# Performance work log

Hardware: AMD Instinct MI355X
Metric: run time of the kernel (lower is better)

Reference implementation:

```python
import jax, jax.numpy as jnp
import numpy as np

B, H = 65536, 128
NUM_LAW, NUM_ACCU, NUM_TIME = 103, 119, 11


def _lstm_cell(x, h, c, Wx, Wh, b):
    # Keras LSTMCell: gates ordered i, f, g, o along last dim of [*, 4H]
    z = x @ Wx + h @ Wh + b
    i, f, g, o = jnp.split(z, 4, axis=-1)
    c_new = jax.nn.sigmoid(f) * c + jax.nn.sigmoid(i) * jnp.tanh(g)
    h_new = jax.nn.sigmoid(o) * jnp.tanh(c_new)
    return h_new, c_new


def setup_inputs() -> dict:
    key = jax.random.key(0)
    ks = jax.random.split(key, 16)
    s = 0.05
    return {
        "x": jax.random.normal(ks[0], (B, H), jnp.float32),
        "Wx": jax.random.normal(ks[1], (3, H, 4 * H), jnp.float32) * s,
        "Wh": jax.random.normal(ks[2], (3, H, 4 * H), jnp.float32) * s,
        "b": jax.random.normal(ks[3], (3, 4 * H), jnp.float32) * s,
        "hfc_W": jax.random.normal(ks[4], (H, H), jnp.float32) * s,
        "hfc_b": jax.random.normal(ks[5], (H,), jnp.float32) * s,
        "cfc_W": jax.random.normal(ks[6], (H, H), jnp.float32) * s,
        "cfc_b": jax.random.normal(ks[7], (H,), jnp.float32) * s,
        "mid_W": jax.random.normal(ks[8], (3, H, H), jnp.float32) * s,
        "mid_b": jax.random.normal(ks[9], (3, H), jnp.float32) * s,
        "out1_W": jax.random.normal(ks[10], (H, NUM_LAW), jnp.float32) * s,
        "out1_b": jax.random.normal(ks[11], (NUM_LAW,), jnp.float32) * s,
        "out2_W": jax.random.normal(ks[12], (H, NUM_ACCU), jnp.float32) * s,
        "out2_b": jax.random.normal(ks[13], (NUM_ACCU,), jnp.float32) * s,
        "out3_W": jax.random.normal(ks[14], (H, NUM_TIME), jnp.float32) * s,
        "out3_b": jax.random.normal(ks[15], (NUM_TIME,), jnp.float32) * s,
    }


def reference(x, Wx, Wh, b, hfc_W, hfc_b, cfc_W, cfc_b, mid_W, mid_b,
              out1_W, out1_b, out2_W, out2_b, out3_W, out3_b):
    zeros = jnp.zeros((B, H), x.dtype)
    # task 1 (law): starts from zero state
    h1, c1 = _lstm_cell(x, zeros, zeros, Wx[0], Wh[0], b[0])
    # graph edges (1,2),(1,3): first visit -> state copied directly (no Dense)
    # task 2 (accu): state = (h1, c1)
    h2, c2 = _lstm_cell(x, h1, c1, Wx[1], Wh[1], b[1])
    # edge (2,3): non-first -> additive dense fusion into task-3 state
    h3_in = h1 + h2 @ hfc_W + hfc_b
    c3_in = c1 + c2 @ cfc_W + cfc_b
    # task 3 (time)
    h3, c3 = _lstm_cell(x, h3_in, c3_in, Wx[2], Wh[2], b[2])
    # more_fc=True head: outfc(relu(midfc(h)))
    o1 = jax.nn.relu(h1 @ mid_W[0] + mid_b[0]) @ out1_W + out1_b
    o2 = jax.nn.relu(h2 @ mid_W[1] + mid_b[1]) @ out2_W + out2_b
    o3 = jax.nn.relu(h3 @ mid_W[2] + mid_b[2]) @ out3_W + out3_b
    return (o1, o2, o3)
```

## Files before the change

### kernel.cpp

```cpp
#include <hip/hip_runtime.h>


#define L2E 1.4426950408889634f

typedef _Float16 half8 __attribute__((ext_vector_type(8)));
typedef float f32x4 __attribute__((ext_vector_type(4)));

#define FWX0 0
#define FWX1 8192
#define FWH1 16384
#define FWX2 24576
#define FWH2 32768
#define FHFC 40960
#define FCFC 43008
#define FMID0 45056
#define FMID1 47104
#define FMID2 49152
#define FOUT1 51200
#define FOUT2 52992
#define FOUT3 55040
#define NBLOB_F16 442368

__global__ void lstm_prep(const float* __restrict__ Wx, const float* __restrict__ Wh,
                          const float* __restrict__ hfcW, const float* __restrict__ cfcW,
                          const float* __restrict__ midW, const float* __restrict__ o1W,
                          const float* __restrict__ o2W, const float* __restrict__ o3W,
                          _Float16* __restrict__ blob)
{
    int idx = blockIdx.x * 256 + threadIdx.x;
    if (idx >= NBLOB_F16) return;

    const float* src;
    int style;
    int N = 0;
    int local;
    if      (idx < FWX1 * 8)  { src = Wx;           local = idx - FWX0 * 8;  style = 0; }
    else if (idx < FWH1 * 8)  { src = Wx + 65536;   local = idx - FWX1 * 8;  style = 0; }
    else if (idx < FWX2 * 8)  { src = Wh + 65536;   local = idx - FWH1 * 8;  style = 0; }
    else if (idx < FWH2 * 8)  { src = Wx + 131072;  local = idx - FWX2 * 8;  style = 0; }
    else if (idx < FHFC * 8)  { src = Wh + 131072;  local = idx - FWH2 * 8;  style = 0; }
    else if (idx < FCFC * 8)  { src = hfcW;         local = idx - FHFC * 8;  style = 1; }
    else if (idx < FMID0 * 8) { src = cfcW;         local = idx - FCFC * 8;  style = 1; }
    else if (idx < FMID1 * 8) { src = midW;         local = idx - FMID0 * 8; style = 1; }
    else if (idx < FMID2 * 8) { src = midW + 16384; local = idx - FMID1 * 8; style = 1; }
    else if (idx < FOUT1 * 8) { src = midW + 32768; local = idx - FMID2 * 8; style = 1; }
    else if (idx < FOUT2 * 8) { src = o1W;          local = idx - FOUT1 * 8; style = 2; N = 103; }
    else if (idx < FOUT3 * 8) { src = o2W;          local = idx - FOUT2 * 8; style = 2; N = 119; }
    else                      { src = o3W;          local = idx - FOUT3 * 8; style = 2; N = 11;  }

    int Mtile = local >> 11;
    int rem   = local & 2047;
    int kb    = rem >> 9;
    int lane  = (rem >> 3) & 63;
    int j     = rem & 7;
    int g = lane >> 4, m = lane & 15;
    int k = 32 * kb + ((j < 4) ? (4 * g + j) : (16 + 4 * g + (j - 4)));

    float v;
    if (style == 0) {
        int ft = Mtile >> 2, gate = Mtile & 3;
        int n = gate * 128 + ft * 16 + m;
        float s = (gate == 2) ? (2.0f * L2E) : (-L2E);
        v = src[k * 512 + n] * s;
    } else if (style == 1) {
        v = src[k * 128 + Mtile * 16 + m];
    } else {
        int n = Mtile * 16 + m;
        v = (n < N) ? src[k * N + n] : 0.0f;
    }
    blob[idx] = (_Float16)v;
}


__device__ __forceinline__ half8 ldA(const _Float16* __restrict__ blob, int base, int frag, int lane)
{
    return ((const half8*)blob)[base + frag * 64 + lane];
}

__device__ __forceinline__ half8 ldX(const float* __restrict__ xrow)
{
    const float4* p = (const float4*)xrow;
    float4 a = p[0];
    float4 b = p[4];
    half8 r;
    r[0] = (_Float16)a.x; r[1] = (_Float16)a.y; r[2] = (_Float16)a.z; r[3] = (_Float16)a.w;
    r[4] = (_Float16)b.x; r[5] = (_Float16)b.y; r[6] = (_Float16)b.z; r[7] = (_Float16)b.w;
    return r;
}

__device__ __forceinline__ float sigz(float z)
{
    return __builtin_amdgcn_rcpf(1.0f + __builtin_amdgcn_exp2f(z));
}

#define MFMA16(A, B, C) __builtin_amdgcn_mfma_f32_16x16x32_f16(A, B, C, 0, 0, 0)

__device__ __forceinline__ void stageA(const _Float16* __restrict__ blob, const float* __restrict__ b3,
                                       const half8 (&xf)[4], half8 (&ho)[4], half8 (&co)[4],
                                       int lane, int rowg)
{
#pragma unroll
    for (int ft = 0; ft < 8; ++ft) {
        f32x4 ai{0,0,0,0}, ag{0,0,0,0}, ao{0,0,0,0};
#pragma unroll
        for (int kb = 0; kb < 4; ++kb) {
            half8 A0 = ldA(blob, FWX0, (ft * 4 + 0) * 4 + kb, lane);
            half8 A2 = ldA(blob, FWX0, (ft * 4 + 2) * 4 + kb, lane);
            half8 A3 = ldA(blob, FWX0, (ft * 4 + 3) * 4 + kb, lane);
            ai = MFMA16(A0, xf[kb], ai);
            ag = MFMA16(A2, xf[kb], ag);
            ao = MFMA16(A3, xf[kb], ao);
        }
        float4 bi4 = *(const float4*)(b3 + 0   + ft * 16 + 4 * rowg);
        float4 bg4 = *(const float4*)(b3 + 256 + ft * 16 + 4 * rowg);
        float4 bo4 = *(const float4*)(b3 + 384 + ft * 16 + 4 * rowg);
        float bi[4] = {bi4.x, bi4.y, bi4.z, bi4.w};
        float bg[4] = {bg4.x, bg4.y, bg4.z, bg4.w};
        float bo[4] = {bo4.x, bo4.y, bo4.z, bo4.w};
#pragma unroll
        for (int r = 0; r < 4; ++r) {
            float si = sigz(ai[r] - L2E * bi[r]);
            float tg = 1.0f - 2.0f * sigz(ag[r] + 2.0f * L2E * bg[r]);
            float so = sigz(ao[r] - L2E * bo[r]);
            float c  = si * tg;
            float h  = so * (1.0f - 2.0f * sigz(2.0f * L2E * c));
            ho[ft >> 1][(ft & 1) * 4 + r] = (_Float16)h;
            co[ft >> 1][(ft & 1) * 4 + r] = (_Float16)c;
        }
    }
}

template <int L, bool WRITE_C>
__device__ __forceinline__ void zstage(const _Float16* __restrict__ blob, const float* __restrict__ b3,
                                       int FX, int FH,
                                       const half8 (&xf)[4], const half8 (&hf)[4],
                                       const half8 (&cp)[4],
                                       half8 (&ho)[4], half8 (&co)[4],
                                       int lane, int rowg)
{
#pragma unroll
    for (int ft = 0; ft < 8; ++ft) {
        f32x4 ai{0,0,0,0}, af{0,0,0,0}, ag{0,0,0,0}, ao{0,0,0,0};
#pragma unroll
        for (int kb = 0; kb < 4; ++kb) {
            half8 A0 = ldA(blob, FX, (ft * 4 + 0) * 4 + kb, lane);
            half8 A1 = ldA(blob, FX, (ft * 4 + 1) * 4 + kb, lane);
            half8 A2 = ldA(blob, FX, (ft * 4 + 2) * 4 + kb, lane);
            half8 A3 = ldA(blob, FX, (ft * 4 + 3) * 4 + kb, lane);
            ai = MFMA16(A0, xf[kb], ai);
            af = MFMA16(A1, xf[kb], af);
            ag = MFMA16(A2, xf[kb], ag);
            ao = MFMA16(A3, xf[kb], ao);
            half8 B0 = ldA(blob, FH, (ft * 4 + 0) * 4 + kb, lane);
            half8 B1 = ldA(blob, FH, (ft * 4 + 1) * 4 + kb, lane);
            half8 B2 = ldA(blob, FH, (ft * 4 + 2) * 4 + kb, lane);
            half8 B3 = ldA(blob, FH, (ft * 4 + 3) * 4 + kb, lane);
            ai = MFMA16(B0, hf[kb], ai);
            af = MFMA16(B1, hf[kb], af);
            ag = MFMA16(B2, hf[kb], ag);
            ao = MFMA16(B3, hf[kb], ao);
        }
        const float* bb = b3 + L * 512;
        float4 bi4 = *(const float4*)(bb + 0   + ft * 16 + 4 * rowg);
        float4 bf4 = *(const float4*)(bb + 128 + ft * 16 + 4 * rowg);
        float4 bg4 = *(const float4*)(bb + 256 + ft * 16 + 4 * rowg);
        float4 bo4 = *(const float4*)(bb + 384 + ft * 16 + 4 * rowg);
        float bi[4] = {bi4.x, bi4.y, bi4.z, bi4.w};
        float bf[4] = {bf4.x, bf4.y, bf4.z, bf4.w};
        float bg[4] = {bg4.x, bg4.y, bg4.z, bg4.w};
        float bo[4] = {bo4.x, bo4.y, bo4.z, bo4.w};
#pragma unroll
        for (int r = 0; r < 4; ++r) {
            float cprev = (float)cp[ft >> 1][(ft & 1) * 4 + r];
            float si = sigz(ai[r] - L2E * bi[r]);
            float sf = sigz(af[r] - L2E * bf[r]);
            float tg = 1.0f - 2.0f * sigz(ag[r] + 2.0f * L2E * bg[r]);
            float so = sigz(ao[r] - L2E * bo[r]);
            float c  = sf * cprev + si * tg;
            float h  = so * (1.0f - 2.0f * sigz(2.0f * L2E * c));
            ho[ft >> 1][(ft & 1) * 4 + r] = (_Float16)h;
            if (WRITE_C) co[ft >> 1][(ft & 1) * 4 + r] = (_Float16)c;
        }
    }
}

__device__ __forceinline__ void fcstage(const _Float16* __restrict__ blob, int FW,
                                        const float* __restrict__ fcb,
                                        const half8 (&bfr)[4], half8 (&io)[4],
                                        int lane, int rowg)
{
#pragma unroll
    for (int ft = 0; ft < 8; ++ft) {
        f32x4 acc{0,0,0,0};
#pragma unroll
        for (int kb = 0; kb < 4; ++kb) {
            half8 A = ldA(blob, FW, ft * 4 + kb, lane);
            acc = MFMA16(A, bfr[kb], acc);
        }
        float4 b4 = *(const float4*)(fcb + ft * 16 + 4 * rowg);
        float bbv[4] = {b4.x, b4.y, b4.z, b4.w};
#pragma unroll
        for (int r = 0; r < 4; ++r) {
            float v = acc[r] + bbv[r] + (float)io[ft >> 1][(ft & 1) * 4 + r];
            io[ft >> 1][(ft & 1) * 4 + r] = (_Float16)v;
        }
    }
}

template <int NMT>
__device__ __forceinline__ void head(const _Float16* __restrict__ blob, int FMID, int FOUT,
                                     const float* __restrict__ midb, const float* __restrict__ outb,
                                     int Nreal, float* __restrict__ outbase, int rowlen,
                                     const half8 (&hf)[4], half8 (&mfr)[4],
                                     int lane, int rowg, int col, int batch0)
{
#pragma unroll
    for (int ft = 0; ft < 8; ++ft) {
        f32x4 acc{0,0,0,0};
#pragma unroll
        for (int kb = 0; kb < 4; ++kb) {
            half8 A = ldA(blob, FMID, ft * 4 + kb, lane);
            acc = MFMA16(A, hf[kb], acc);
        }
        float4 b4 = *(const float4*)(midb + ft * 16 + 4 * rowg);
        float mb[4] = {b4.x, b4.y, b4.z, b4.w};
#pragma unroll
        for (int r = 0; r < 4; ++r) {
            float mv = fmaxf(acc[r] + mb[r], 0.0f);
            mfr[ft >> 1][(ft & 1) * 4 + r] = (_Float16)mv;
        }
    }
    int batch = batch0 + col;
#pragma unroll
    for (int Mt = 0; Mt < NMT; ++Mt) {
        f32x4 acc{0,0,0,0};
#pragma unroll
        for (int kb = 0; kb < 4; ++kb) {
            half8 A = ldA(blob, FOUT, Mt * 4 + kb, lane);
            acc = MFMA16(A, mfr[kb], acc);
        }
#pragma unroll
        for (int r = 0; r < 4; ++r) {
            int n = Mt * 16 + 4 * rowg + r;
            if (n < Nreal)
                outbase[batch * rowlen + n] = acc[r] + outb[n];
        }
    }
}

__global__ __launch_bounds__(256, 2) void lstm_fused(
    const float* __restrict__ x, const float* __restrict__ b3,
    const float* __restrict__ hfc_b, const float* __restrict__ cfc_b,
    const float* __restrict__ mid_b, const float* __restrict__ o1b,
    const float* __restrict__ o2b, const float* __restrict__ o3b,
    const _Float16* __restrict__ blob, float* __restrict__ out)
{
    int tid = threadIdx.x;
    int lane = tid & 63;
    int wv = tid >> 6;
    int wave = blockIdx.x * 4 + wv;
    int batch0 = wave * 16;
    int rowg = lane >> 4, col = lane & 15;

    half8 xf[4], hA[4], cA[4], hB[4], cB[4], mfr[4];

#pragma unroll
    for (int kb = 0; kb < 4; ++kb)
        xf[kb] = ldX(x + (size_t)(batch0 + col) * 128 + 32 * kb + 4 * rowg);

    stageA(blob, b3, xf, hA, cA, lane, rowg);
    head<7>(blob, FMID0, FOUT1, mid_b, o1b, 103, out, 103, hA, mfr, lane, rowg, col, batch0);
    zstage<1, true>(blob, b3, FWX1, FWH1, xf, hA, cA, hB, cB, lane, rowg);
    fcstage(blob, FHFC, hfc_b, hB, hA, lane, rowg);
    fcstage(blob, FCFC, cfc_b, cB, cA, lane, rowg);
    head<8>(blob, FMID1, FOUT2, mid_b + 128, o2b, 119, out + (size_t)65536 * 103, 119, hB, mfr, lane, rowg, col, batch0);
    zstage<2, false>(blob, b3, FWX2, FWH2, xf, hA, cA, hB, cB, lane, rowg);
    head<1>(blob, FMID2, FOUT3, mid_b + 256, o3b, 11, out + (size_t)65536 * 222, 11, hB, mfr, lane, rowg, col, batch0);
}

extern "C" void kernel_launch(void* const* d_in, const int* in_sizes, int n_in,
                              void* d_out, int out_size, void* d_ws, size_t ws_size,
                              hipStream_t stream)
{
    const float* x     = (const float*)d_in[0];
    const float* Wx    = (const float*)d_in[1];
    const float* Wh    = (const float*)d_in[2];
    const float* b3    = (const float*)d_in[3];
    const float* hfcW  = (const float*)d_in[4];
    const float* hfc_b = (const float*)d_in[5];
    const float* cfcW  = (const float*)d_in[6];
    const float* cfc_b = (const float*)d_in[7];
    const float* midW  = (const float*)d_in[8];
    const float* mid_b = (const float*)d_in[9];
    const float* o1W   = (const float*)d_in[10];
    const float* o1b   = (const float*)d_in[11];
    const float* o2W   = (const float*)d_in[12];
    const float* o2b   = (const float*)d_in[13];
    const float* o3W   = (const float*)d_in[14];
    const float* o3b   = (const float*)d_in[15];
    float* out = (float*)d_out;

    if (ws_size < (size_t)NBLOB_F16 * sizeof(_Float16)) return;
    _Float16* blob = (_Float16*)d_ws;

    lstm_prep<<<(NBLOB_F16 + 255) / 256, 256, 0, stream>>>(Wx, Wh, hfcW, cfcW, midW, o1W, o2W, o3W, blob);
    lstm_fused<<<1024, 256, 0, stream>>>(x, b3, hfc_b, cfc_b, mid_b, o1b, o2b, o3b, blob, out);
}
```

Measured before the change: 321.6 us.

## Switch to 32x32 MFMA and stream weights through double-buffered LDS

Moves all GEMMs from 16x16x32 to 32x32x16 MFMA tiles, with each wave handling 32 batch rows instead of 16, and re-lays out the fp16 weight blob to match. Weight fragments are no longer read from global memory by every wave. Instead they go through a 55-phase schedule that prefetches the next phase into a double-buffered LDS region with global_load_lds, separated by block barriers. This is meant to cut redundant global/L2 weight traffic and raise MFMA efficiency. The cost is a barrier per phase, heavy register use (launch bounds drop to 1 block per CU) and half as many blocks.

```diff
diff --git a/kernel.cpp b/kernel.cpp
--- a/kernel.cpp
+++ b/kernel.cpp
@@ -4,7 +4,7 @@
 #define L2E 1.4426950408889634f
 
 typedef _Float16 half8 __attribute__((ext_vector_type(8)));
-typedef float f32x4 __attribute__((ext_vector_type(4)));
+typedef float f32x16 __attribute__((ext_vector_type(16)));
 
 #define FWX0 0
 #define FWX1 8192
@@ -17,9 +17,13 @@
 #define FMID1 47104
 #define FMID2 49152
 #define FOUT1 51200
-#define FOUT2 52992
-#define FOUT3 55040
-#define NBLOB_F16 442368
+#define FOUT2 53248
+#define FOUT3 55296
+#define NBLOB_H8 55808
+#define NBLOB_F16 446464
+
+#define MFMA32(A, B, C) __builtin_amdgcn_mfma_f32_32x32x16_f16(A, B, C, 0, 0, 0)
+#define ZERO16 f32x16{0,0,0,0,0,0,0,0,0,0,0,0,0,0,0,0}
 
 __global__ void lstm_prep(const float* __restrict__ Wx, const float* __restrict__ Wh,
                           const float* __restrict__ hfcW, const float* __restrict__ cfcW,
@@ -30,252 +34,309 @@
     int idx = blockIdx.x * 256 + threadIdx.x;
     if (idx >= NBLOB_F16) return;
 
+    int frag = idx >> 9;
+    int rem  = idx & 511;
+    int lane = rem >> 3;
+    int j    = rem & 7;
+    int m    = lane & 31;
+    int g    = lane >> 5;
+    int kin  = (j & 3) + 8 * (j >> 2) + 4 * g;
+
     const float* src;
-    int style;
-    int N = 0;
-    int local;
-    if      (idx < FWX1 * 8)  { src = Wx;           local = idx - FWX0 * 8;  style = 0; }
-    else if (idx < FWH1 * 8)  { src = Wx + 65536;   local = idx - FWX1 * 8;  style = 0; }
-    else if (idx < FWX2 * 8)  { src = Wh + 65536;   local = idx - FWH1 * 8;  style = 0; }
-    else if (idx < FWH2 * 8)  { src = Wx + 131072;  local = idx - FWX2 * 8;  style = 0; }
-    else if (idx < FHFC * 8)  { src = Wh + 131072;  local = idx - FWH2 * 8;  style = 0; }
-    else if (idx < FCFC * 8)  { src = hfcW;         local = idx - FHFC * 8;  style = 1; }
-    else if (idx < FMID0 * 8) { src = cfcW;         local = idx - FCFC * 8;  style = 1; }
-    else if (idx < FMID1 * 8) { src = midW;         local = idx - FMID0 * 8; style = 1; }
-    else if (idx < FMID2 * 8) { src = midW + 16384; local = idx - FMID1 * 8; style = 1; }
-    else if (idx < FOUT1 * 8) { src = midW + 32768; local = idx - FMID2 * 8; style = 1; }
-    else if (idx < FOUT2 * 8) { src = o1W;          local = idx - FOUT1 * 8; style = 2; N = 103; }
-    else if (idx < FOUT3 * 8) { src = o2W;          local = idx - FOUT2 * 8; style = 2; N = 119; }
-    else                      { src = o3W;          local = idx - FOUT3 * 8; style = 2; N = 11;  }
-
-    int Mtile = local >> 11;
-    int rem   = local & 2047;
-    int kb    = rem >> 9;
-    int lane  = (rem >> 3) & 63;
-    int j     = rem & 7;
-    int g = lane >> 4, m = lane & 15;
-    int k = 32 * kb + ((j < 4) ? (4 * g + j) : (16 + 4 * g + (j - 4)));
+    int style, N = 0, lf;
+    if      (frag < 128) { src = Wx;            lf = frag;       style = 0; }
+    else if (frag < 256) { src = Wx + 65536;    lf = frag - 128; style = 0; }
+    else if (frag < 384) { src = Wh + 65536;    lf = frag - 256; style = 0; }
+    else if (frag < 512) { src = Wx + 131072;   lf = frag - 384; style = 0; }
+    else if (frag < 640) { src = Wh + 131072;   lf = frag - 512; style = 0; }
+    else if (frag < 672) { src = hfcW;          lf = frag - 640; style = 1; }
+    else if (frag < 704) { src = cfcW;          lf = frag - 672; style = 1; }
+    else if (frag < 736) { src = midW;          lf = frag - 704; style = 1; }
+    else if (frag < 768) { src = midW + 16384;  lf = frag - 736; style = 1; }
+    else if (frag < 800) { src = midW + 32768;  lf = frag - 768; style = 1; }
+    else if (frag < 832) { src = o1W;           lf = frag - 800; style = 2; N = 103; }
+    else if (frag < 864) { src = o2W;           lf = frag - 832; style = 2; N = 119; }
+    else                 { src = o3W;           lf = frag - 864; style = 2; N = 11;  }
 
     float v;
     if (style == 0) {
-        int ft = Mtile >> 2, gate = Mtile & 3;
-        int n = gate * 128 + ft * 16 + m;
+        int mt = lf >> 5, gate = (lf >> 3) & 3, kc = lf & 7;
+        int k = kc * 16 + kin;
+        int n = gate * 128 + mt * 32 + m;
         float s = (gate == 2) ? (2.0f * L2E) : (-L2E);
         v = src[k * 512 + n] * s;
     } else if (style == 1) {
-        v = src[k * 128 + Mtile * 16 + m];
+        int mt = lf >> 3, kc = lf & 7;
+        v = src[(kc * 16 + kin) * 128 + mt * 32 + m];
     } else {
-        int n = Mtile * 16 + m;
-        v = (n < N) ? src[k * N + n] : 0.0f;
+        int mt = lf >> 3, kc = lf & 7;
+        int n = mt * 32 + m;
+        v = (n < N) ? src[(kc * 16 + kin) * N + n] : 0.0f;
     }
     blob[idx] = (_Float16)v;
 }
 
 
-__device__ __forceinline__ half8 ldA(const _Float16* __restrict__ blob, int base, int frag, int lane)
-{
-    return ((const half8*)blob)[base + frag * 64 + lane];
-}
-
-__device__ __forceinline__ half8 ldX(const float* __restrict__ xrow)
-{
-    const float4* p = (const float4*)xrow;
-    float4 a = p[0];
-    float4 b = p[4];
-    half8 r;
-    r[0] = (_Float16)a.x; r[1] = (_Float16)a.y; r[2] = (_Float16)a.z; r[3] = (_Float16)a.w;
-    r[4] = (_Float16)b.x; r[5] = (_Float16)b.y; r[6] = (_Float16)b.z; r[7] = (_Float16)b.w;
-    return r;
-}
-
 __device__ __forceinline__ float sigz(float z)
 {
     return __builtin_amdgcn_rcpf(1.0f + __builtin_amdgcn_exp2f(z));
 }
 
-#define MFMA16(A, B, C) __builtin_amdgcn_mfma_f32_16x16x32_f16(A, B, C, 0, 0, 0)
-
-__device__ __forceinline__ void stageA(const _Float16* __restrict__ blob, const float* __restrict__ b3,
-                                       const half8 (&xf)[4], half8 (&ho)[4], half8 (&co)[4],
-                                       int lane, int rowg)
-{
-#pragma unroll
-    for (int ft = 0; ft < 8; ++ft) {
-        f32x4 ai{0,0,0,0}, ag{0,0,0,0}, ao{0,0,0,0};
-#pragma unroll
-        for (int kb = 0; kb < 4; ++kb) {
-            half8 A0 = ldA(blob, FWX0, (ft * 4 + 0) * 4 + kb, lane);
-            half8 A2 = ldA(blob, FWX0, (ft * 4 + 2) * 4 + kb, lane);
-            half8 A3 = ldA(blob, FWX0, (ft * 4 + 3) * 4 + kb, lane);
-            ai = MFMA16(A0, xf[kb], ai);
-            ag = MFMA16(A2, xf[kb], ag);
-            ao = MFMA16(A3, xf[kb], ao);
-        }
-        float4 bi4 = *(const float4*)(b3 + 0   + ft * 16 + 4 * rowg);
-        float4 bg4 = *(const float4*)(b3 + 256 + ft * 16 + 4 * rowg);
-        float4 bo4 = *(const float4*)(b3 + 384 + ft * 16 + 4 * rowg);
-        float bi[4] = {bi4.x, bi4.y, bi4.z, bi4.w};
-        float bg[4] = {bg4.x, bg4.y, bg4.z, bg4.w};
-        float bo[4] = {bo4.x, bo4.y, bo4.z, bo4.w};
-#pragma unroll
-        for (int r = 0; r < 4; ++r) {
-            float si = sigz(ai[r] - L2E * bi[r]);
-            float tg = 1.0f - 2.0f * sigz(ag[r] + 2.0f * L2E * bg[r]);
-            float so = sigz(ao[r] - L2E * bo[r]);
-            float c  = si * tg;
-            float h  = so * (1.0f - 2.0f * sigz(2.0f * L2E * c));
-            ho[ft >> 1][(ft & 1) * 4 + r] = (_Float16)h;
-            co[ft >> 1][(ft & 1) * 4 + r] = (_Float16)c;
-        }
-    }
-}
-
-template <int L, bool WRITE_C>
-__device__ __forceinline__ void zstage(const _Float16* __restrict__ blob, const float* __restrict__ b3,
-                                       int FX, int FH,
-                                       const half8 (&xf)[4], const half8 (&hf)[4],
-                                       const half8 (&cp)[4],
-                                       half8 (&ho)[4], half8 (&co)[4],
-                                       int lane, int rowg)
-{
-#pragma unroll
-    for (int ft = 0; ft < 8; ++ft) {
-        f32x4 ai{0,0,0,0}, af{0,0,0,0}, ag{0,0,0,0}, ao{0,0,0,0};
-#pragma unroll
-        for (int kb = 0; kb < 4; ++kb) {
-            half8 A0 = ldA(blob, FX, (ft * 4 + 0) * 4 + kb, lane);
-            half8 A1 = ldA(blob, FX, (ft * 4 + 1) * 4 + kb, lane);
-            half8 A2 = ldA(blob, FX, (ft * 4 + 2) * 4 + kb, lane);
-            half8 A3 = ldA(blob, FX, (ft * 4 + 3) * 4 + kb, lane);
-            ai = MFMA16(A0, xf[kb], ai);
-            af = MFMA16(A1, xf[kb], af);
-            ag = MFMA16(A2, xf[kb], ag);
-            ao = MFMA16(A3, xf[kb], ao);
-            half8 B0 = ldA(blob, FH, (ft * 4 + 0) * 4 + kb, lane);
-            half8 B1 = ldA(blob, FH, (ft * 4 + 1) * 4 + kb, lane);
-            half8 B2 = ldA(blob, FH, (ft * 4 + 2) * 4 + kb, lane);
-            half8 B3 = ldA(blob, FH, (ft * 4 + 3) * 4 + kb, lane);
-            ai = MFMA16(B0, hf[kb], ai);
-            af = MFMA16(B1, hf[kb], af);
-            ag = MFMA16(B2, hf[kb], ag);
-            ao = MFMA16(B3, hf[kb], ao);
-        }
-        const float* bb = b3 + L * 512;
-        float4 bi4 = *(const float4*)(bb + 0   + ft * 16 + 4 * rowg);
-        float4 bf4 = *(const float4*)(bb + 128 + ft * 16 + 4 * rowg);
-        float4 bg4 = *(const float4*)(bb + 256 + ft * 16 + 4 * rowg);
-        float4 bo4 = *(const float4*)(bb + 384 + ft * 16 + 4 * rowg);
-        float bi[4] = {bi4.x, bi4.y, bi4.z, bi4.w};
-        float bf[4] = {bf4.x, bf4.y, bf4.z, bf4.w};
-        float bg[4] = {bg4.x, bg4.y, bg4.z, bg4.w};
-        float bo[4] = {bo4.x, bo4.y, bo4.z, bo4.w};
-#pragma unroll
-        for (int r = 0; r < 4; ++r) {
-            float cprev = (float)cp[ft >> 1][(ft & 1) * 4 + r];
-            float si = sigz(ai[r] - L2E * bi[r]);
-            float sf = sigz(af[r] - L2E * bf[r]);
-            float tg = 1.0f - 2.0f * sigz(ag[r] + 2.0f * L2E * bg[r]);
-            float so = sigz(ao[r] - L2E * bo[r]);
-            float c  = sf * cprev + si * tg;
-            float h  = so * (1.0f - 2.0f * sigz(2.0f * L2E * c));
-            ho[ft >> 1][(ft & 1) * 4 + r] = (_Float16)h;
-            if (WRITE_C) co[ft >> 1][(ft & 1) * 4 + r] = (_Float16)c;
-        }
-    }
-}
-
-__device__ __forceinline__ void fcstage(const _Float16* __restrict__ blob, int FW,
-                                        const float* __restrict__ fcb,
-                                        const half8 (&bfr)[4], half8 (&io)[4],
-                                        int lane, int rowg)
-{
-#pragma unroll
-    for (int ft = 0; ft < 8; ++ft) {
-        f32x4 acc{0,0,0,0};
-#pragma unroll
-        for (int kb = 0; kb < 4; ++kb) {
-            half8 A = ldA(blob, FW, ft * 4 + kb, lane);
-            acc = MFMA16(A, bfr[kb], acc);
-        }
-        float4 b4 = *(const float4*)(fcb + ft * 16 + 4 * rowg);
-        float bbv[4] = {b4.x, b4.y, b4.z, b4.w};
-#pragma unroll
-        for (int r = 0; r < 4; ++r) {
-            float v = acc[r] + bbv[r] + (float)io[ft >> 1][(ft & 1) * 4 + r];
-            io[ft >> 1][(ft & 1) * 4 + r] = (_Float16)v;
-        }
-    }
-}
-
-template <int NMT>
-__device__ __forceinline__ void head(const _Float16* __restrict__ blob, int FMID, int FOUT,
-                                     const float* __restrict__ midb, const float* __restrict__ outb,
-                                     int Nreal, float* __restrict__ outbase, int rowlen,
-                                     const half8 (&hf)[4], half8 (&mfr)[4],
-                                     int lane, int rowg, int col, int batch0)
-{
-#pragma unroll
-    for (int ft = 0; ft < 8; ++ft) {
-        f32x4 acc{0,0,0,0};
-#pragma unroll
-        for (int kb = 0; kb < 4; ++kb) {
-            half8 A = ldA(blob, FMID, ft * 4 + kb, lane);
-            acc = MFMA16(A, hf[kb], acc);
-        }
-        float4 b4 = *(const float4*)(midb + ft * 16 + 4 * rowg);
-        float mb[4] = {b4.x, b4.y, b4.z, b4.w};
-#pragma unroll
-        for (int r = 0; r < 4; ++r) {
-            float mv = fmaxf(acc[r] + mb[r], 0.0f);
-            mfr[ft >> 1][(ft & 1) * 4 + r] = (_Float16)mv;
-        }
-    }
-    int batch = batch0 + col;
-#pragma unroll
-    for (int Mt = 0; Mt < NMT; ++Mt) {
-        f32x4 acc{0,0,0,0};
-#pragma unroll
-        for (int kb = 0; kb < 4; ++kb) {
-            half8 A = ldA(blob, FOUT, Mt * 4 + kb, lane);
-            acc = MFMA16(A, mfr[kb], acc);
-        }
-#pragma unroll
-        for (int r = 0; r < 4; ++r) {
-            int n = Mt * 16 + 4 * rowg + r;
-            if (n < Nreal)
-                outbase[batch * rowlen + n] = acc[r] + outb[n];
-        }
-    }
-}
-
-__global__ __launch_bounds__(256, 2) void lstm_fused(
+__device__ __forceinline__ void phase_of(int p, int& b, int& n)
+{
+    n = 16;
+    if (p < 8)        b = FWX0 + (p >> 1) * 2048 + (p & 1) * 1024;
+    else if (p < 10)  b = FMID0 + (p - 8) * 1024;
+    else if (p < 12)  b = FOUT1 + (p - 10) * 1024;
+    else if (p < 28) { int q = p - 12, mt = q >> 2, sb = q & 3;
+                       b = ((sb & 2) ? FWH1 : FWX1) + mt * 2048 + (sb & 1) * 1024; }
+    else if (p < 30)  b = FHFC + (p - 28) * 1024;
+    else if (p < 32)  b = FCFC + (p - 30) * 1024;
+    else if (p < 34)  b = FMID1 + (p - 32) * 1024;
+    else if (p < 36)  b = FOUT2 + (p - 34) * 1024;
+    else if (p < 52) { int q = p - 36, mt = q >> 2, sb = q & 3;
+                       b = ((sb & 2) ? FWH2 : FWX2) + mt * 2048 + (sb & 1) * 1024; }
+    else if (p < 54)  b = FMID2 + (p - 52) * 1024;
+    else if (p == 54) { b = FOUT3; n = 8; }
+    else             { b = 0; n = 0; }
+}
+
+__device__ __forceinline__ void stage_phase(const _Float16* __restrict__ blob, int base_h8, int nfrags,
+                                            _Float16* dst, int wv, int lane)
+{
+    const char* gbase = (const char*)((const half8*)blob + base_h8);
+    auto* d = (__attribute__((address_space(3))) char*)dst;
+#pragma unroll
+    for (int i = 0; i < 4; ++i) {
+        int f = i * 4 + wv;
+        if (f < nfrags) {
+            __builtin_amdgcn_global_load_lds(
+                (const __attribute__((address_space(1))) void*)(gbase + (size_t)(f * 64 + lane) * 16),
+                (__attribute__((address_space(3))) void*)(d + f * 1024), 16, 0, 0);
+        }
+    }
+}
+
+#define STEP_BEGIN { int nb_, nn_; phase_of(p + 1, nb_, nn_);                     \
+                     if (nn_) stage_phase(blob, nb_, nn_, lds + (cur ^ 1) * 8192, wv, lane); \
+                     const _Float16* Lb = lds + cur * 8192;
+#define STEP_END     __syncthreads(); cur ^= 1; ++p; }
+#define LDS_FRAG(fl) (((const half8*)Lb)[(fl) * 64 + lane])
+
+__global__ __launch_bounds__(256, 1) void lstm_fused(
     const float* __restrict__ x, const float* __restrict__ b3,
     const float* __restrict__ hfc_b, const float* __restrict__ cfc_b,
     const float* __restrict__ mid_b, const float* __restrict__ o1b,
     const float* __restrict__ o2b, const float* __restrict__ o3b,
     const _Float16* __restrict__ blob, float* __restrict__ out)
 {
-    int tid = threadIdx.x;
-    int lane = tid & 63;
-    int wv = tid >> 6;
-    int wave = blockIdx.x * 4 + wv;
-    int batch0 = wave * 16;
-    int rowg = lane >> 4, col = lane & 15;
-
-    half8 xf[4], hA[4], cA[4], hB[4], cB[4], mfr[4];
-
-#pragma unroll
-    for (int kb = 0; kb < 4; ++kb)
-        xf[kb] = ldX(x + (size_t)(batch0 + col) * 128 + 32 * kb + 4 * rowg);
-
-    stageA(blob, b3, xf, hA, cA, lane, rowg);
-    head<7>(blob, FMID0, FOUT1, mid_b, o1b, 103, out, 103, hA, mfr, lane, rowg, col, batch0);
-    zstage<1, true>(blob, b3, FWX1, FWH1, xf, hA, cA, hB, cB, lane, rowg);
-    fcstage(blob, FHFC, hfc_b, hB, hA, lane, rowg);
-    fcstage(blob, FCFC, cfc_b, cB, cA, lane, rowg);
-    head<8>(blob, FMID1, FOUT2, mid_b + 128, o2b, 119, out + (size_t)65536 * 103, 119, hB, mfr, lane, rowg, col, batch0);
-    zstage<2, false>(blob, b3, FWX2, FWH2, xf, hA, cA, hB, cB, lane, rowg);
-    head<1>(blob, FMID2, FOUT3, mid_b + 256, o3b, 11, out + (size_t)65536 * 222, 11, hB, mfr, lane, rowg, col, batch0);
+    __shared__ _Float16 lds[16384];
+
+    int tid = threadIdx.x, lane = tid & 63, wv = tid >> 6;
+    int g = lane >> 5;
+    int batch = blockIdx.x * 128 + wv * 32 + (lane & 31);
+
+    half8 xf[8], hA[8], cA[8], hB[8], cB[8], mfr[8];
+
+#pragma unroll
+    for (int kc = 0; kc < 8; ++kc) {
+        const float* xr = x + (size_t)batch * 128 + kc * 16 + 4 * g;
+        float4 a = *(const float4*)xr;
+        float4 b = *(const float4*)(xr + 8);
+        half8 v;
+        v[0]=(_Float16)a.x; v[1]=(_Float16)a.y; v[2]=(_Float16)a.z; v[3]=(_Float16)a.w;
+        v[4]=(_Float16)b.x; v[5]=(_Float16)b.y; v[6]=(_Float16)b.z; v[7]=(_Float16)b.w;
+        xf[kc] = v;
+    }
+
+    int p = 0, cur = 0;
+    { int b0, n0; phase_of(0, b0, n0); stage_phase(blob, b0, n0, lds, wv, lane); }
+    __syncthreads();
+
+    auto head_mid = [&](const half8 (&hf)[8], const float* midbp) {
+#pragma unroll
+        for (int g2 = 0; g2 < 2; ++g2) {
+            STEP_BEGIN
+#pragma unroll
+            for (int mtl = 0; mtl < 2; ++mtl) {
+                const int mt = 2 * g2 + mtl;
+                f32x16 acc = ZERO16;
+#pragma unroll
+                for (int kc = 0; kc < 8; ++kc) acc = MFMA32(LDS_FRAG(mtl * 8 + kc), hf[kc], acc);
+#pragma unroll
+                for (int t = 0; t < 4; ++t) {
+                    float4 B4 = *(const float4*)(midbp + mt * 32 + 8 * t + 4 * g);
+                    float bv[4] = {B4.x, B4.y, B4.z, B4.w};
+#pragma unroll
+                    for (int s = 0; s < 4; ++s) {
+                        const int q = 4 * t + s;
+                        float mv = fmaxf(acc[q] + bv[s], 0.0f);
+                        if (q < 8) mfr[2 * mt][q] = (_Float16)mv; else mfr[2 * mt + 1][q - 8] = (_Float16)mv;
+                    }
+                }
+            }
+            STEP_END
+        }
+    };
+
+    auto head_out2 = [&](int Nreal, float* obase, int rowlen, const float* outb) {
+#pragma unroll
+        for (int g2 = 0; g2 < 2; ++g2) {
+            STEP_BEGIN
+#pragma unroll
+            for (int mtl = 0; mtl < 2; ++mtl) {
+                const int mt = 2 * g2 + mtl;
+                f32x16 acc = ZERO16;
+#pragma unroll
+                for (int kc = 0; kc < 8; ++kc) acc = MFMA32(LDS_FRAG(mtl * 8 + kc), mfr[kc], acc);
+#pragma unroll
+                for (int t = 0; t < 4; ++t)
+#pragma unroll
+                    for (int s = 0; s < 4; ++s) {
+                        const int q = 4 * t + s;
+                        int n = mt * 32 + 8 * t + 4 * g + s;
+                        if (n < Nreal) obase[(size_t)batch * rowlen + n] = acc[q] + outb[n];
+                    }
+            }
+            STEP_END
+        }
+    };
+
+    auto fc_f = [&](const half8 (&bfr)[8], half8 (&io)[8], const float* fcb) {
+#pragma unroll
+        for (int g2 = 0; g2 < 2; ++g2) {
+            STEP_BEGIN
+#pragma unroll
+            for (int mtl = 0; mtl < 2; ++mtl) {
+                const int mt = 2 * g2 + mtl;
+                f32x16 acc = ZERO16;
+#pragma unroll
+                for (int kc = 0; kc < 8; ++kc) acc = MFMA32(LDS_FRAG(mtl * 8 + kc), bfr[kc], acc);
+#pragma unroll
+                for (int t = 0; t < 4; ++t) {
+                    float4 B4 = *(const float4*)(fcb + mt * 32 + 8 * t + 4 * g);
+                    float bv[4] = {B4.x, B4.y, B4.z, B4.w};
+#pragma unroll
+                    for (int s = 0; s < 4; ++s) {
+                        const int q = 4 * t + s;
+                        float prev = (q < 8) ? (float)io[2 * mt][q] : (float)io[2 * mt + 1][q - 8];
+                        float v = acc[q] + bv[s] + prev;
+                        if (q < 8) io[2 * mt][q] = (_Float16)v; else io[2 * mt + 1][q - 8] = (_Float16)v;
+                    }
+                }
+            }
+            STEP_END
+        }
+    };
+
+    auto zstage_f = [&](const half8 (&hf)[8], const half8 (&cp)[8],
+                        half8 (&ho)[8], half8 (&co)[8], const float* bb, bool writeC) {
+#pragma unroll
+        for (int mt = 0; mt < 4; ++mt) {
+            f32x16 ai = ZERO16, af = ZERO16, agg = ZERO16, ao = ZERO16;
+            STEP_BEGIN
+#pragma unroll
+            for (int kc = 0; kc < 8; ++kc) { ai = MFMA32(LDS_FRAG(kc), xf[kc], ai);
+                                             af = MFMA32(LDS_FRAG(8 + kc), xf[kc], af); }
+            STEP_END
+            STEP_BEGIN
+#pragma unroll
+            for (int kc = 0; kc < 8; ++kc) { agg = MFMA32(LDS_FRAG(kc), xf[kc], agg);
+                                             ao  = MFMA32(LDS_FRAG(8 + kc), xf[kc], ao); }
+            STEP_END
+            STEP_BEGIN
+#pragma unroll
+            for (int kc = 0; kc < 8; ++kc) { ai = MFMA32(LDS_FRAG(kc), hf[kc], ai);
+                                             af = MFMA32(LDS_FRAG(8 + kc), hf[kc], af); }
+            STEP_END
+            STEP_BEGIN
+#pragma unroll
+            for (int kc = 0; kc < 8; ++kc) { agg = MFMA32(LDS_FRAG(kc), hf[kc], agg);
+                                             ao  = MFMA32(LDS_FRAG(8 + kc), hf[kc], ao); }
+#pragma unroll
+            for (int t = 0; t < 4; ++t) {
+                float4 Bi = *(const float4*)(bb + 0   + mt * 32 + 8 * t + 4 * g);
+                float4 Bf = *(const float4*)(bb + 128 + mt * 32 + 8 * t + 4 * g);
+                float4 Bg = *(const float4*)(bb + 256 + mt * 32 + 8 * t + 4 * g);
+                float4 Bo = *(const float4*)(bb + 384 + mt * 32 + 8 * t + 4 * g);
+                float bi[4]={Bi.x,Bi.y,Bi.z,Bi.w}, bf[4]={Bf.x,Bf.y,Bf.z,Bf.w};
+                float bg[4]={Bg.x,Bg.y,Bg.z,Bg.w}, bo[4]={Bo.x,Bo.y,Bo.z,Bo.w};
+#pragma unroll
+                for (int s = 0; s < 4; ++s) {
+                    const int q = 4 * t + s;
+                    float cprev = (q < 8) ? (float)cp[2 * mt][q] : (float)cp[2 * mt + 1][q - 8];
+                    float si = sigz(ai[q] - L2E * bi[s]);
+                    float sf = sigz(af[q] - L2E * bf[s]);
+                    float tg = 1.0f - 2.0f * sigz(agg[q] + 2.0f * L2E * bg[s]);
+                    float so = sigz(ao[q] - L2E * bo[s]);
+                    float c  = sf * cprev + si * tg;
+                    float h  = so * (1.0f - 2.0f * sigz(2.0f * L2E * c));
+                    if (q < 8) ho[2 * mt][q] = (_Float16)h; else ho[2 * mt + 1][q - 8] = (_Float16)h;
+                    if (writeC) { if (q < 8) co[2 * mt][q] = (_Float16)c; else co[2 * mt + 1][q - 8] = (_Float16)c; }
+                }
+            }
+            STEP_END
+        }
+    };
+
+#pragma unroll
+    for (int mt = 0; mt < 4; ++mt) {
+        f32x16 ai = ZERO16, agg = ZERO16, ao = ZERO16;
+        STEP_BEGIN
+#pragma unroll
+        for (int kc = 0; kc < 8; ++kc) ai = MFMA32(LDS_FRAG(kc), xf[kc], ai);
+        STEP_END
+        STEP_BEGIN
+#pragma unroll
+        for (int kc = 0; kc < 8; ++kc) { agg = MFMA32(LDS_FRAG(kc), xf[kc], agg);
+                                         ao  = MFMA32(LDS_FRAG(8 + kc), xf[kc], ao); }
+#pragma unroll
+        for (int t = 0; t < 4; ++t) {
+            float4 Bi = *(const float4*)(b3 + 0   + mt * 32 + 8 * t + 4 * g);
+            float4 Bg = *(const float4*)(b3 + 256 + mt * 32 + 8 * t + 4 * g);
+            float4 Bo = *(const float4*)(b3 + 384 + mt * 32 + 8 * t + 4 * g);
+            float bi[4]={Bi.x,Bi.y,Bi.z,Bi.w}, bg[4]={Bg.x,Bg.y,Bg.z,Bg.w}, bo[4]={Bo.x,Bo.y,Bo.z,Bo.w};
+#pragma unroll
+            for (int s = 0; s < 4; ++s) {
+                const int q = 4 * t + s;
+                float si = sigz(ai[q] - L2E * bi[s]);
+                float tg = 1.0f - 2.0f * sigz(agg[q] + 2.0f * L2E * bg[s]);
+                float so = sigz(ao[q] - L2E * bo[s]);
+                float c  = si * tg;
+                float h  = so * (1.0f - 2.0f * sigz(2.0f * L2E * c));
+                if (q < 8) { hA[2 * mt][q] = (_Float16)h; cA[2 * mt][q] = (_Float16)c; }
+                else       { hA[2 * mt + 1][q - 8] = (_Float16)h; cA[2 * mt + 1][q - 8] = (_Float16)c; }
+            }
+        }
+        STEP_END
+    }
+
+    head_mid(hA, mid_b);
+    head_out2(103, out, 103, o1b);
+    zstage_f(hA, cA, hB, cB, b3 + 512, true);
+    fc_f(hB, hA, hfc_b);
+    fc_f(cB, cA, cfc_b);
+    head_mid(hB, mid_b + 128);
+    head_out2(119, out + (size_t)65536 * 103, 119, o2b);
+    zstage_f(hA, cA, hB, cB, b3 + 1024, false);
+    head_mid(hB, mid_b + 256);
+
+    STEP_BEGIN
+    {
+        f32x16 acc = ZERO16;
+#pragma unroll
+        for (int kc = 0; kc < 8; ++kc) acc = MFMA32(LDS_FRAG(kc), mfr[kc], acc);
+        float* obase = out + (size_t)65536 * 222;
+#pragma unroll
+        for (int t = 0; t < 4; ++t)
+#pragma unroll
+            for (int s = 0; s < 4; ++s) {
+                const int q = 4 * t + s;
+                int n = 8 * t + 4 * g + s;
+                if (n < 11) obase[(size_t)batch * 11 + n] = acc[q] + o3b[n];
+            }
+    }
+    STEP_END
 }
 
 extern "C" void kernel_launch(void* const* d_in, const int* in_sizes, int n_in,
@@ -303,6 +364,6 @@
     if (ws_size < (size_t)NBLOB_F16 * sizeof(_Float16)) return;
     _Float16* blob = (_Float16*)d_ws;
 
-    lstm_prep<<<(NBLOB_F16 + 255) / 256, 256, 0, stream>>>(Wx, Wh, hfcW, cfcW, midW, o1W, o2W, o3W, blob);
-    lstm_fused<<<1024, 256, 0, stream>>>(x, b3, hfc_b, cfc_b, mid_b, o1b, o2b, o3b, blob, out);
-}
+    lstm_prep<<<NBLOB_F16 / 256, 256, 0, stream>>>(Wx, Wh, hfcW, cfcW, midW, o1W, o2W, o3W, blob);
+    lstm_fused<<<512, 256, 0, stream>>>(x, b3, hfc_b, cfc_b, mid_b, o1b, o2b, o3b, blob, out);
+}
```

Result: slower. 470.7 us (+46.4%).
